# Optimization experiments

Measured on AMD Instinct MI355X. Metric: run time of the kernel, lower is better.

## Reference

```python
import jax, jax.numpy as jnp
import numpy as np

# dims: recurrence runs over axis 0 (B steps), cell batch is T (faithful to the
# original code, which unpacks `length, batch_size, _ = input.size()` on a
# batch-first tensor).
B, T, D = 32, 2048, 256
H = 512 // 2          # per-direction hidden (hidden_dim // 2)
CS = 32               # chunk_size
N = H // CS           # n_chunk = 8
G = 4 * H + 2 * N     # gate width = 1040


def setup_inputs() -> dict:
    key = jax.random.key(0)
    ks = jax.random.split(key, 5)
    x = jax.random.normal(ks[0], (B, T, D), jnp.float32)
    # seq_lens: sorted int lengths in [1, T] (concrete numpy -> static gather)
    sl = np.sort(np.random.default_rng(0).integers(1, T + 1, size=B)).astype(np.int64)
    s_in = 1.0 / np.sqrt(D)
    s_h = 1.0 / np.sqrt(H)
    W_ih = jax.random.uniform(ks[1], (G, D), jnp.float32, -s_in, s_in)
    b_ih = jax.random.uniform(ks[2], (G,), jnp.float32, -s_in, s_in)
    W_hh = jax.random.uniform(ks[3], (G, H), jnp.float32, -s_h, s_h)
    b_hh = jax.random.uniform(ks[4], (G,), jnp.float32, -s_h, s_h)
    return {"embedded_text": x, "seq_lens": sl,
            "W_ih": W_ih, "b_ih": b_ih, "W_hh": W_hh, "b_hh": b_hh}


def _cumsoftmax(x):
    return jnp.cumsum(jax.nn.softmax(x, axis=-1), axis=-1)


def _run_onlstm(x, W_ih, b_ih, W_hh, b_hh):
    """x: (B, T, D) -> hidden states (B, T, H); scan over axis 0."""
    t_in = jnp.einsum('btd,gd->btg', x, W_ih) + b_ih  # precomputed ih, (B,T,G)
    h0 = jnp.zeros((T, H), x.dtype)
    c0 = jnp.zeros((T, N, CS), x.dtype)

    def step(carry, ti):
        hx, cx = carry
        gates = ti + hx @ W_hh.T + b_hh                 # (T, G)
        cin = 1.0 - _cumsoftmax(gates[:, :N])           # (T, N)
        cfg = _cumsoftmax(gates[:, N:2 * N])            # (T, N)
        rest = gates[:, 2 * N:].reshape(-1, 4 * N, CS)
        og, cg, ig, fg = jnp.split(rest, 4, axis=1)     # each (T, N, CS)
        ig = jax.nn.sigmoid(ig)
        fg = jax.nn.sigmoid(fg)
        cg = jnp.tanh(cg)
        og = jax.nn.sigmoid(og)
        cin3 = cin[:, :, None]
        cfg3 = cfg[:, :, None]
        ov = cfg3 * cin3
        fg = fg * ov + (cfg3 - ov)
        ig = ig * ov + (cin3 - ov)
        cy = fg * cx + ig * cg
        hy = (og * jnp.tanh(cy)).reshape(-1, H)
        return (hy, cy), hy

    _, hs = jax.lax.scan(step, (h0, c0), t_in)          # (B, T, H)
    return hs


def reference(embedded_text, seq_lens, W_ih, b_ih, W_hh, b_hh):
    # eval mode: nn.Dropout / LockedDropout are identity; dropconnect=0 -> plain weight
    out_f = _run_onlstm(embedded_text, W_ih, b_ih, W_hh, b_hh)
    # faithful quirk: 'bidirectional' pass flips the FEATURE dim, same weights
    out_b = _run_onlstm(embedded_text[..., ::-1], W_ih, b_ih, W_hh, b_hh)
    out = jnp.concatenate([out_f, out_b], axis=-1)      # (B, T, 2H)
    sl = np.asarray(seq_lens)
    rows = np.repeat(np.arange(sl.shape[0]), sl)
    cols = np.concatenate([np.arange(int(l)) for l in sl])
    return out[rows, cols]                              # (sum(seq_lens), 2H)
```

## Files before the change

kernel.cpp:

```cpp
#include <hip/hip_runtime.h>
#include <hip/hip_bf16.h>

#define B_  32
#define T_  2048
#define D_  256
#define H_  256
#define G_  1040

#define NSL 8
#define NRB 16
#define NMB 4
#define NKB 32
#define NF  5
#define CTRSTRIDE 64

using bf16   = __hip_bfloat16;
using short8 = __attribute__((ext_vector_type(8))) short;
using f32x16 = __attribute__((ext_vector_type(16))) float;
using ull    = unsigned long long;

__device__ inline float sigmoidf_(float v) {
  return __fdividef(1.f, 1.f + __expf(-v));
}
__device__ inline float tanh_(float v) {
  v = fminf(fmaxf(v, -15.f), 15.f);
  float e = __expf(2.f * v);
  return __fdividef(e - 1.f, e + 1.f);
}
__device__ inline float bf2f(unsigned short u) {
  union { unsigned int i; float f; } c; c.i = ((unsigned int)u) << 16; return c.f;
}
__device__ inline float ldF(const void* p, size_t i, int isf) {
  return isf ? ((const float*)p)[i] : bf2f(((const unsigned short*)p)[i]);
}
__device__ inline short f2bs(float v) {
  bf16 h = __float2bfloat16(v);
  return *(short*)&h;
}

__global__ __launch_bounds__(256) void detect_prep(
    const unsigned short* __restrict__ xh, const int* __restrict__ sli,
    int* __restrict__ meta)
{
  __shared__ int s_bad;
  if (threadIdx.x == 0) s_bad = 0;
  __syncthreads();
  int bad = 0;
  for (int i = threadIdx.x; i < 1024; i += 256) {
    float f = bf2f(xh[i]);
    if (!(fabsf(f) < 100.f)) bad = 1;
  }
  if (bad) atomicOr(&s_bad, 1);
  __syncthreads();
  if (threadIdx.x == 0) {
    meta[0] = s_bad;
    bool is64 = true;
    for (int i = 1; i < 32; i += 2) if (sli[i] != 0) is64 = false;
    int base = 0;
    for (int b = 0; b < B_; ++b) {
      int v = is64 ? sli[2 * b] : sli[b];
      meta[8 + b]  = v;
      meta[40 + b] = base;
      base += v;
    }
  }
}

__global__ __launch_bounds__(256) void build_bsum(
    const void* __restrict__ b_ih, const void* __restrict__ b_hh,
    float* __restrict__ bsum, const int* __restrict__ meta)
{
  const int isf = meta[0];
  int i = blockIdx.x * 256 + threadIdx.x;
  if (i < G_) bsum[i] = ldF(b_ih, i, isf) + ldF(b_hh, i, isf);
}

__global__ __launch_bounds__(256) void build_xs(
    const void* __restrict__ x, bf16* __restrict__ xs,
    const int* __restrict__ meta)
{
  const int isf = meta[0];
  size_t idx = (size_t)blockIdx.x * 256 + threadIdx.x;
  if (idx >= (size_t)B_ * T_ * D_ / 8) return;
  const int b  = (int)(idx >> 16);
  const int r  = (int)(idx & 65535);
  const int t  = r >> 5;
  const int kc = r & 31;
  const size_t src = ((size_t)b * T_ + t) * D_ + kc * 8;
  short8 v;
  #pragma unroll
  for (int j = 0; j < 8; ++j) v[j] = f2bs(ldF(x, src + j, isf));
  const int rb = t >> 7, mb = (t >> 5) & 3, trow = t & 31;
  const int kbx = kc >> 1, k8 = kc & 1;
  const size_t off = ((((size_t)b * 16 + rb) * 16 + kbx) * 4 + mb) * 64
                     + (k8 * 32 + trow);
  *(short8*)(xs + off * 8) = v;
}

__global__ __launch_bounds__(256) void build_wsw(
    const void* __restrict__ W_ih, const void* __restrict__ W_hh,
    bf16* __restrict__ Wsw, const int* __restrict__ meta)
{
  const int isf = meta[0];
  int idx = blockIdx.x * 256 + threadIdx.x;
  if (idx >= 2 * NSL * NKB * NF * 64) return;
  const int lane = idx & 63;
  const int f    = (idx >> 6) % NF;
  const int kb   = (idx / (64 * NF)) % NKB;
  const int sl   = (idx / (64 * NF * NKB)) % NSL;
  const int d    = idx / (64 * NF * NKB * NSL);
  const int n    = lane & 31;
  const int k0   = kb * 16 + (lane >> 5) * 8;
  const int g = (f < 4) ? (16 + f * H_ + sl * 32 + n) : ((n < 16) ? n : -1);
  short8 v;
  #pragma unroll
  for (int j = 0; j < 8; ++j) {
    float val = 0.f;
    const int k = k0 + j;
    if (g >= 0)
      val = (k < D_) ? ldF(W_ih, (size_t)g * D_ + (d ? (D_ - 1 - k) : k), isf)
                     : ldF(W_hh, (size_t)g * H_ + (k - D_), isf);
    v[j] = f2bs(val);
  }
  *(short8*)(Wsw + (size_t)idx * 8) = v;
}

__global__ __launch_bounds__(256, 1) void onlstm_persist(
    const short* __restrict__ xs, const short* __restrict__ Wsw,
    short* __restrict__ hs, float* __restrict__ cs,
    const float* __restrict__ bsum, void* __restrict__ out,
    const int* __restrict__ meta, int* __restrict__ ctr,
    int b_lo, int b_hi)
{
  __shared__ short Wl[NKB * 4 * 512];
  __shared__ __align__(16) short Ht[NMB][32][40];

  const int tid  = threadIdx.x;
  const int lane = tid & 63;
  const int w    = tid >> 6;

  const int lin = blockIdx.x;
  const int rb  = (lin & 7) + 8 * ((lin >> 3) >> 4);
  const int p   = (lin >> 3) & 15;
  const int d   = p >> 3;
  const int s   = p & 7;

  const int col   = lane & 31;
  const int khalf = lane >> 5;
  const int isf   = meta[0];

  const short* wsrc = Wsw + ((size_t)(d * NSL + s) * NKB) * (NF * 512);

  for (int i = tid; i < NKB * 4 * 64; i += 256) {
    const int kb = i >> 8, rem = i & 255, f = rem >> 6, l = rem & 63;
    *(short8*)&Wl[((kb * 4 + f) << 9) + (l << 3)] =
        *(const short8*)(wsrc + ((kb * 5 + f) << 9) + (l << 3));
  }
  __syncthreads();

  float bg[4];
  #pragma unroll
  for (int f = 0; f < 4; ++f) bg[f] = bsum[16 + f * H_ + s * 32 + col];
  const float c0b = (col < 16) ? bsum[col] : 0.f;

  const int e = s * 32 + col;

  int* gctr = ctr + (size_t)(d * NRB + rb) * CTRSTRIDE;
  const short* w4p = wsrc + 4 * 512 + lane * 8;

  float* csP = cs + (((size_t)(d * NSL + s) * NRB + rb) * NMB + w) * 1024 + lane;

  f32x16 creg;
  if (b_lo > 0) {
    #pragma unroll
    for (int r = 0; r < 16; ++r) creg[r] = csP[r * 64];
  } else {
    #pragma unroll
    for (int r = 0; r < 16; ++r) creg[r] = 0.f;
  }

  for (int b = b_lo; b < b_hi; ++b) {
    const int len_s  = meta[8 + b];
    const int base_s = meta[40 + b];

    f32x16 acc[NF];
    #pragma unroll
    for (int f = 0; f < NF; ++f)
      #pragma unroll
      for (int r = 0; r < 16; ++r) acc[f][r] = 0.f;

    {
      const short* aPtr = xs + (((size_t)b * NRB + rb) * 16 * NMB + w) * 512 + lane * 8;
      const short* w4q  = w4p;
      short8 a0 = *(const short8*)(aPtr);
      short8 a1 = *(const short8*)(aPtr + 2048);
      short8 a2 = *(const short8*)(aPtr + 4096);
      short8 q0 = *(const short8*)(w4q);
      short8 q1 = *(const short8*)(w4q + 2560);
      short8 q2 = *(const short8*)(w4q + 5120);
      #pragma unroll
      for (int kb = 0; kb < 16; ++kb) {
        const short8 af = a0, b4 = q0;
        a0 = a1; a1 = a2; q0 = q1; q1 = q2;
        if (kb < 13) {
          a2 = *(const short8*)(aPtr + (kb + 3) * 2048);
          q2 = *(const short8*)(w4q + (kb + 3) * 2560);
        }
        #pragma unroll
        for (int f = 0; f < 4; ++f) {
          const short8 bfr = *(const short8*)&Wl[((kb * 4 + f) << 9) + (lane << 3)];
          acc[f] = __builtin_amdgcn_mfma_f32_32x32x16_bf16(af, bfr, acc[f], 0, 0, 0);
        }
        acc[4] = __builtin_amdgcn_mfma_f32_32x32x16_bf16(af, b4, acc[4], 0, 0, 0);
      }
    }

    if (b) {
      if (tid == 0) {
        ull t0 = __builtin_amdgcn_s_memrealtime();
        while (__hip_atomic_load(gctr, __ATOMIC_RELAXED,
                                 __HIP_MEMORY_SCOPE_AGENT) < 8 * b) {
          __builtin_amdgcn_s_sleep(1);
          if (__builtin_amdgcn_s_memrealtime() - t0 > 40000000ull) break;
        }
      }
      __syncthreads();

      ull hfA[16], hfB[16];
      {
        const short* hbase = hs + (((size_t)(((b & 1) ^ 1) * 2 + d) * NRB + rb) * 16 * NMB + w) * 512;
        #pragma unroll
        for (int kb = 0; kb < 16; ++kb) {
          const ull* p = (const ull*)(hbase + (size_t)kb * NMB * 512) + lane * 2;
          hfA[kb] = __hip_atomic_load(p,     __ATOMIC_RELAXED, __HIP_MEMORY_SCOPE_AGENT);
          hfB[kb] = __hip_atomic_load(p + 1, __ATOMIC_RELAXED, __HIP_MEMORY_SCOPE_AGENT);
        }
      }

      const short* w4q = w4p + 16 * 2560;
      short8 q0 = *(const short8*)(w4q);
      short8 q1 = *(const short8*)(w4q + 2560);
      short8 q2 = *(const short8*)(w4q + 5120);
      #pragma unroll
      for (int kb = 0; kb < 16; ++kb) {
        union { ull u[2]; short8 v; } af;
        af.u[0] = hfA[kb]; af.u[1] = hfB[kb];
        const short8 b4 = q0;
        q0 = q1; q1 = q2;
        if (kb < 13) q2 = *(const short8*)(w4q + (kb + 3) * 2560);
        #pragma unroll
        for (int f = 0; f < 4; ++f) {
          const short8 bfr = *(const short8*)&Wl[(((16 + kb) * 4 + f) << 9) + (lane << 3)];
          acc[f] = __builtin_amdgcn_mfma_f32_32x32x16_bf16(af.v, bfr, acc[f], 0, 0, 0);
        }
        acc[4] = __builtin_amdgcn_mfma_f32_32x32x16_bf16(af.v, b4, acc[4], 0, 0, 0);
      }
    }

    f32x16 gv, mx, Sv, Pv;
    #pragma unroll
    for (int r = 0; r < 16; ++r) gv[r] = acc[4][r] + c0b;
    #pragma unroll
    for (int r = 0; r < 16; ++r) mx[r] = gv[r];
    #pragma unroll
    for (int r = 0; r < 16; ++r) { float t = __shfl_xor(mx[r], 1); mx[r] = fmaxf(mx[r], t); }
    #pragma unroll
    for (int r = 0; r < 16; ++r) { float t = __shfl_xor(mx[r], 2); mx[r] = fmaxf(mx[r], t); }
    #pragma unroll
    for (int r = 0; r < 16; ++r) { float t = __shfl_xor(mx[r], 4); mx[r] = fmaxf(mx[r], t); }
    #pragma unroll
    for (int r = 0; r < 16; ++r) gv[r] = __expf(gv[r] - mx[r]);
    const bool pin = (lane & 7) <= s;
    #pragma unroll
    for (int r = 0; r < 16; ++r) { Sv[r] = gv[r]; Pv[r] = pin ? gv[r] : 0.f; }
    #pragma unroll
    for (int r = 0; r < 16; ++r) { Sv[r] += __shfl_xor(Sv[r], 1); Pv[r] += __shfl_xor(Pv[r], 1); }
    #pragma unroll
    for (int r = 0; r < 16; ++r) { Sv[r] += __shfl_xor(Sv[r], 2); Pv[r] += __shfl_xor(Pv[r], 2); }
    #pragma unroll
    for (int r = 0; r < 16; ++r) { Sv[r] += __shfl_xor(Sv[r], 4); Pv[r] += __shfl_xor(Pv[r], 4); }
    #pragma unroll
    for (int r = 0; r < 16; ++r) Pv[r] = __fdividef(Pv[r], Sv[r]);
    f32x16 cinv, cfgv;
    #pragma unroll
    for (int r = 0; r < 16; ++r) cinv[r] = 1.f - __shfl(Pv[r], khalf * 32);
    #pragma unroll
    for (int r = 0; r < 16; ++r) cfgv[r] = __shfl(Pv[r], khalf * 32 + 8);

    #pragma unroll
    for (int r = 0; r < 16; ++r) {
      const int row = (r & 3) + 8 * (r >> 2) + 4 * khalf;
      const float cin = cinv[r];
      const float cfg = cfgv[r];
      const float og = sigmoidf_(acc[0][r] + bg[0]);
      const float cg = tanh_   (acc[1][r] + bg[1]);
      const float ig = sigmoidf_(acc[2][r] + bg[2]);
      const float fg = sigmoidf_(acc[3][r] + bg[3]);
      const float ov = cfg * cin;
      const float f2 = fg * ov + (cfg - ov);
      const float i2 = ig * ov + (cin - ov);
      const float cy = f2 * creg[r] + i2 * cg;
      creg[r] = cy;
      const float hy = og * tanh_(cy);
      Ht[w][row][col] = f2bs(hy);
      const int t = rb * 128 + w * 32 + row;
      if (t < len_s) {
        const size_t o = (size_t)(base_s + t) * (2 * H_) + (size_t)d * H_ + e;
        if (isf) ((float*)out)[o] = hy;
        else     ((bf16*)out)[o]  = __float2bfloat16(hy);
      }
    }

    {
      const int m  = lane & 31;
      const int k8 = lane >> 5;
      short* hbase = hs + (((size_t)((b & 1) * 2 + d) * NRB + rb) * 16 * NMB + w) * 512;
      #pragma unroll
      for (int c = 0; c < 2; ++c) {
        ull lo = *(const ull*)&Ht[w][m][c * 16 + k8 * 8];
        ull hi = *(const ull*)&Ht[w][m][c * 16 + k8 * 8 + 4];
        ull* q = (ull*)(hbase + (size_t)(2 * s + c) * NMB * 512) + lane * 2;
        __hip_atomic_store(q,     lo, __ATOMIC_RELAXED, __HIP_MEMORY_SCOPE_AGENT);
        __hip_atomic_store(q + 1, hi, __ATOMIC_RELAXED, __HIP_MEMORY_SCOPE_AGENT);
      }
    }

    __syncthreads();
    if (tid == 0)
      __hip_atomic_fetch_add(gctr, 1, __ATOMIC_RELAXED, __HIP_MEMORY_SCOPE_AGENT);
  }

  if (b_hi < B_) {
    #pragma unroll
    for (int r = 0; r < 16; ++r) csP[r * 64] = creg[r];
  }
}

extern "C" void kernel_launch(void* const* d_in, const int* in_sizes, int n_in,
                              void* d_out, int out_size, void* d_ws, size_t ws_size,
                              hipStream_t stream)
{
  const void* x    = d_in[0];
  const int*  sl   = (const int*)d_in[1];
  const void* W_ih = d_in[2];
  const void* b_ih = d_in[3];
  const void* W_hh = d_in[4];
  const void* b_hh = d_in[5];

  char* ws = (char*)d_ws;
  size_t off = 0;
  auto alloc = [&](size_t bytes) {
    void* p = ws + off;
    off = (off + bytes + 255) & ~(size_t)255;
    return p;
  };
  int*   meta = (int*)  alloc(128 * sizeof(int));
  short* xs   = (short*)alloc((size_t)B_ * T_ * D_ * sizeof(short));
  short* Wsw  = (short*)alloc((size_t)2 * NSL * NKB * NF * 512 * sizeof(short));
  short* hs   = (short*)alloc((size_t)2 * 2 * T_ * H_ * sizeof(short));
  float* bsum = (float*)alloc((size_t)G_ * sizeof(float));
  int*   ctr  = (int*)  alloc((size_t)32 * CTRSTRIDE * sizeof(int));
  float* cs   = (float*)alloc((size_t)2 * NSL * NRB * NMB * 1024 * sizeof(float));
  const bool have_cs = (off <= ws_size);

  hipMemsetAsync(hs, 0, (size_t)2 * 2 * T_ * H_ * sizeof(short), stream);
  hipMemsetAsync(ctr, 0, (size_t)32 * CTRSTRIDE * sizeof(int), stream);

  detect_prep<<<1, 256, 0, stream>>>((const unsigned short*)x, sl, meta);
  build_bsum<<<(G_ + 255) / 256, 256, 0, stream>>>(b_ih, b_hh, bsum, meta);
  build_xs<<<(int)(((size_t)B_ * T_ * D_ / 8 + 255) / 256), 256, 0, stream>>>(x, (bf16*)xs, meta);
  build_wsw<<<(2 * NSL * NKB * NF * 64 + 255) / 256, 256, 0, stream>>>(W_ih, W_hh, (bf16*)Wsw, meta);

  int b_lo = 0, b_hi = B_;
  void* args[] = {(void*)&xs, (void*)&Wsw, (void*)&hs, (void*)&cs, (void*)&bsum,
                  (void*)&d_out, (void*)&meta, (void*)&ctr, (void*)&b_lo, (void*)&b_hi};
  hipError_t ce = hipLaunchCooperativeKernel((const void*)onlstm_persist,
                                             dim3(256), dim3(256), args, 0, stream);
  if (ce != hipSuccess) {
    (void)hipGetLastError();
    if (have_cs) {
      for (int b = 0; b < B_; ++b)
        onlstm_persist<<<dim3(256), dim3(256), 0, stream>>>(
            xs, Wsw, hs, cs, bsum, d_out, meta, ctr, b, b + 1);
    } else {
      onlstm_persist<<<dim3(256), dim3(256), 0, stream>>>(
          xs, Wsw, hs, cs, bsum, d_out, meta, ctr, 0, B_);
    }
  }
}
```

Baseline: 676.2 us.

## Prefetch next step's input tile into registers across recurrence steps

The x-projection operand tiles for the next batch step are now loaded into a 16-entry register array during the current step's MFMA loop. This replaces the old three-deep in-loop load pipeline, hiding global load latency across the sequential recurrence. The input conversion kernel also gains a vector-load fast path for bf16 input. The cost is 16 extra short8 registers per thread held across the synchronisation wait, which may raise register pressure or lower occupancy.

```diff
diff --git a/kernel.cpp b/kernel.cpp
--- a/kernel.cpp
+++ b/kernel.cpp
@@ -88,8 +88,13 @@
   const int kc = r & 31;
   const size_t src = ((size_t)b * T_ + t) * D_ + kc * 8;
   short8 v;
-  #pragma unroll
-  for (int j = 0; j < 8; ++j) v[j] = f2bs(ldF(x, src + j, isf));
+  if (!isf) {
+    v = *(const short8*)((const unsigned short*)x + src);
+  } else {
+    const float* xf = (const float*)x + src;
+    #pragma unroll
+    for (int j = 0; j < 8; ++j) v[j] = f2bs(xf[j]);
+  }
   const int rb = t >> 7, mb = (t >> 5) & 3, trow = t & 31;
   const int kbx = kc >> 1, k8 = kc & 1;
   const size_t off = ((((size_t)b * 16 + rb) * 16 + kbx) * 4 + mb) * 64
@@ -179,6 +184,14 @@
     for (int r = 0; r < 16; ++r) creg[r] = 0.f;
   }
 
+  short8 xn[16];
+  {
+    const short* aPtr = xs + (((size_t)b_lo * NRB + rb) * 16 * NMB + w) * 512 + lane * 8;
+    #pragma unroll
+    for (int kb = 0; kb < 16; ++kb)
+      xn[kb] = *(const short8*)(aPtr + (size_t)kb * 2048);
+  }
+
   for (int b = b_lo; b < b_hi; ++b) {
     const int len_s  = meta[8 + b];
     const int base_s = meta[40 + b];
@@ -190,22 +203,19 @@
       for (int r = 0; r < 16; ++r) acc[f][r] = 0.f;
 
     {
-      const short* aPtr = xs + (((size_t)b * NRB + rb) * 16 * NMB + w) * 512 + lane * 8;
-      const short* w4q  = w4p;
-      short8 a0 = *(const short8*)(aPtr);
-      short8 a1 = *(const short8*)(aPtr + 2048);
-      short8 a2 = *(const short8*)(aPtr + 4096);
+      const short* aNext = xs + (((size_t)(b + 1) * NRB + rb) * 16 * NMB + w) * 512 + lane * 8;
+      const bool pf = (b + 1 < b_hi);
+      const short* w4q = w4p;
       short8 q0 = *(const short8*)(w4q);
       short8 q1 = *(const short8*)(w4q + 2560);
       short8 q2 = *(const short8*)(w4q + 5120);
       #pragma unroll
       for (int kb = 0; kb < 16; ++kb) {
-        const short8 af = a0, b4 = q0;
-        a0 = a1; a1 = a2; q0 = q1; q1 = q2;
-        if (kb < 13) {
-          a2 = *(const short8*)(aPtr + (kb + 3) * 2048);
-          q2 = *(const short8*)(w4q + (kb + 3) * 2560);
-        }
+        const short8 af = xn[kb];
+        if (pf) xn[kb] = *(const short8*)(aNext + (size_t)kb * 2048);
+        const short8 b4 = q0;
+        q0 = q1; q1 = q2;
+        if (kb < 13) q2 = *(const short8*)(w4q + (kb + 3) * 2560);
         #pragma unroll
         for (int f = 0; f < 4; ++f) {
           const short8 bfr = *(const short8*)&Wl[((kb * 4 + f) << 9) + (lane << 3)];
@@ -231,9 +241,9 @@
         const short* hbase = hs + (((size_t)(((b & 1) ^ 1) * 2 + d) * NRB + rb) * 16 * NMB + w) * 512;
         #pragma unroll
         for (int kb = 0; kb < 16; ++kb) {
-          const ull* p = (const ull*)(hbase + (size_t)kb * NMB * 512) + lane * 2;
-          hfA[kb] = __hip_atomic_load(p,     __ATOMIC_RELAXED, __HIP_MEMORY_SCOPE_AGENT);
-          hfB[kb] = __hip_atomic_load(p + 1, __ATOMIC_RELAXED, __HIP_MEMORY_SCOPE_AGENT);
+          const ull* hp = (const ull*)(hbase + (size_t)kb * NMB * 512) + lane * 2;
+          hfA[kb] = __hip_atomic_load(hp,     __ATOMIC_RELAXED, __HIP_MEMORY_SCOPE_AGENT);
+          hfB[kb] = __hip_atomic_load(hp + 1, __ATOMIC_RELAXED, __HIP_MEMORY_SCOPE_AGENT);
         }
       }
 
```

Result: faster. 626.9 us (-7.3%).
